# Performance work log

Hardware: AMD Instinct MI355X
Metric: run time of the kernel (lower is better)

The kernel has to match this reference:

```python
import jax, jax.numpy as jnp
import numpy as np

VOCAB = 50257
CH = 1024          # c_hidden_size = hidden_size(1020) + class_num(4)
LAT = 128
T = 1024
EOS = 1


def setup_inputs() -> dict:
    key = jax.random.key(0)
    ks = jax.random.split(key, 12)
    s = 0.02
    # tokens in [2, VOCAB) so EOS only appears at the final position
    toks = jax.random.randint(ks[0], (T,), 2, VOCAB, dtype=jnp.int32)
    input_tensor = toks.at[-1].set(EOS)
    inp = {
        "input_tensor": input_tensor,
        "h0": jnp.zeros((1, 1, CH), jnp.float32),
        "c0": jnp.zeros((1, 1, CH), jnp.float32),
        "eps": jax.random.normal(ks[1], (1, 1, LAT), jnp.float32),
        "emb": jax.random.normal(ks[2], (VOCAB, CH), jnp.float32) * s,
        "W_ih": jax.random.normal(ks[3], (4 * CH, CH), jnp.float32) * s,
        "W_hh": jax.random.normal(ks[4], (4 * CH, CH), jnp.float32) * s,
        "b_ih": jax.random.normal(ks[5], (4 * CH,), jnp.float32) * s,
        "b_hh": jax.random.normal(ks[6], (4 * CH,), jnp.float32) * s,
        "W_mean": jax.random.normal(ks[7], (LAT, 2 * CH), jnp.float32) * s,
        "b_mean": jnp.zeros((LAT,), jnp.float32),
        "W_logv": jax.random.normal(ks[8], (LAT, 2 * CH), jnp.float32) * s,
        "b_logv": jnp.zeros((LAT,), jnp.float32),
    }
    return inp


def reference(input_tensor, h0, c0, eps, emb, W_ih, W_hh, b_ih, b_hh,
              W_mean, b_mean, W_logv, b_logv):
    Tlen = input_tensor.shape[0]
    eos_idx = jnp.argmax(input_tensor == EOS)           # first EOS position
    active = jnp.arange(Tlen) < eos_idx                 # steps taken before break
    x_all = emb[input_tensor]                            # [T, CH]

    def step(carry, inp):
        h, c = carry
        x, a = inp
        gates = x @ W_ih.T + b_ih + h @ W_hh.T + b_hh    # [4*CH]
        i, f, g, o = jnp.split(gates, 4)                 # PyTorch LSTM gate order
        c_new = jax.nn.sigmoid(f) * c + jax.nn.sigmoid(i) * jnp.tanh(g)
        h_new = jax.nn.sigmoid(o) * jnp.tanh(c_new)
        h = jnp.where(a, h_new, h)
        c = jnp.where(a, c_new, c)
        return (h, c), None

    (h, c), _ = jax.lax.scan(step, (h0.reshape(-1), c0.reshape(-1)), (x_all, active))
    hc = jnp.concatenate([h, c])                         # cat((h, c), dim=2) flattened
    mean = hc @ W_mean.T + b_mean
    logv = hc @ W_logv.T + b_logv
    z = eps.reshape(-1) * jnp.exp(0.5 * logv) + mean     # reparameterize
    shp = (1, 1, LAT)
    return z.reshape(shp), mean.reshape(shp), logv.reshape(shp)
```

## Files before the change

### kernel.cpp

```cpp
#include <hip/hip_runtime.h>
#include <cstdint>
#include <cstddef>

#define T_LEN 1024
#define CH    1024
#define NGATE 4096
#define LAT   128
#define NBLK  128

#define WS_XG    0
#define WS_HBUF  (16777216)
#define WS_HFIN  (16777216 + 16384)
#define WS_CFIN  (16777216 + 24576)
#define WS_CTRL  (16777216 + 32768)

__device__ __forceinline__ float sigmf(float x) { return 1.0f / (1.0f + expf(-x)); }

__global__ __launch_bounds__(1024) void setup_k(const int* __restrict__ tok,
                                                int* __restrict__ ctrl) {
  __shared__ int red[1024];
  int tid = threadIdx.x;
  red[tid] = (tok[tid] == 1) ? tid : 0x7fffffff;
  __syncthreads();
  for (int s = 512; s > 0; s >>= 1) {
    if (tid < s) red[tid] = min(red[tid], red[tid + s]);
    __syncthreads();
  }
  if (tid == 0) {
    int e = red[0];
    ctrl[0] = (e == 0x7fffffff) ? 0 : e;
  }
}

__global__ __launch_bounds__(512) void xgemm_k(const int* __restrict__ tok,
                                               const float* __restrict__ emb,
                                               const float* __restrict__ Wih,
                                               const float* __restrict__ bih,
                                               const float* __restrict__ bhh,
                                               float* __restrict__ xg) {
  __shared__ float As[16 * 132];
  __shared__ float Bs[16 * 132];
  const int tid = threadIdx.x;
  const int r0 = blockIdx.x * 128;
  const int t0 = blockIdx.y * 128;
  const int tx = tid & 15, ty = tid >> 4;
  const int m0 = ty * 4, n0 = tx * 8;
  const int lrow = tid >> 2;
  const int kq   = (tid & 3) * 4;

  float acc[4][8];
#pragma unroll
  for (int i = 0; i < 4; i++)
#pragma unroll
    for (int j = 0; j < 8; j++) acc[i][j] = 0.0f;

  const int tokv = tok[t0 + lrow];
  const float* arow = emb + (size_t)tokv * CH;
  const float* brow = Wih + (size_t)(r0 + lrow) * CH;

  for (int k0 = 0; k0 < CH; k0 += 16) {
    float4 a4 = *(const float4*)(arow + k0 + kq);
    float4 b4 = *(const float4*)(brow + k0 + kq);
    __syncthreads();
    As[(kq + 0) * 132 + lrow] = a4.x;
    As[(kq + 1) * 132 + lrow] = a4.y;
    As[(kq + 2) * 132 + lrow] = a4.z;
    As[(kq + 3) * 132 + lrow] = a4.w;
    Bs[(kq + 0) * 132 + lrow] = b4.x;
    Bs[(kq + 1) * 132 + lrow] = b4.y;
    Bs[(kq + 2) * 132 + lrow] = b4.z;
    Bs[(kq + 3) * 132 + lrow] = b4.w;
    __syncthreads();
#pragma unroll
    for (int kk = 0; kk < 16; kk++) {
      float4 av = *(const float4*)&As[kk * 132 + m0];
      float4 b0 = *(const float4*)&Bs[kk * 132 + n0];
      float4 b1 = *(const float4*)&Bs[kk * 132 + n0 + 4];
      float aa[4] = {av.x, av.y, av.z, av.w};
      float bb[8] = {b0.x, b0.y, b0.z, b0.w, b1.x, b1.y, b1.z, b1.w};
#pragma unroll
      for (int i = 0; i < 4; i++)
#pragma unroll
        for (int j = 0; j < 8; j++) acc[i][j] += aa[i] * bb[j];
    }
  }

  float4 bi0 = *(const float4*)(bih + r0 + n0);
  float4 bi1 = *(const float4*)(bih + r0 + n0 + 4);
  float4 bh0 = *(const float4*)(bhh + r0 + n0);
  float4 bh1 = *(const float4*)(bhh + r0 + n0 + 4);
  float badd[8] = {bi0.x + bh0.x, bi0.y + bh0.y, bi0.z + bh0.z, bi0.w + bh0.w,
                   bi1.x + bh1.x, bi1.y + bh1.y, bi1.z + bh1.z, bi1.w + bh1.w};
#pragma unroll
  for (int i = 0; i < 4; i++) {
    float4 o0 = {acc[i][0] + badd[0], acc[i][1] + badd[1],
                 acc[i][2] + badd[2], acc[i][3] + badd[3]};
    float4 o1 = {acc[i][4] + badd[4], acc[i][5] + badd[5],
                 acc[i][6] + badd[6], acc[i][7] + badd[7]};
    float* dst = xg + (size_t)(t0 + m0 + i) * NGATE + r0 + n0;
    *(float4*)(dst) = o0;
    *(float4*)(dst + 4) = o1;
  }
}

__global__ __launch_bounds__(1024) void lstm_k(const float* __restrict__ h0,
                                               const float* __restrict__ c0,
                                               const float* __restrict__ eps,
                                               const float* __restrict__ Whh,
                                               const float* __restrict__ Wm,
                                               const float* __restrict__ bm,
                                               const float* __restrict__ Wl,
                                               const float* __restrict__ bl,
                                               const float* __restrict__ xg,
                                               unsigned long long* __restrict__ hbuf64,
                                               unsigned long long* __restrict__ hfin64,
                                               unsigned long long* __restrict__ cfin64,
                                               const int* __restrict__ ctrl,
                                               float* __restrict__ out) {
  __shared__ float hs[1024];
  __shared__ float hcs[2048];
  __shared__ float gv[32];
  __shared__ float rs[32];

  const int tid = threadIdx.x;
  const int b = blockIdx.x;
  const int g = tid >> 5, s = tid & 31;
  const int q = g >> 3, jj = g & 7;
  const int r = q * 1024 + b * 8 + jj;

  const float* wrow = Whh + (size_t)r * CH;
  float w[32];
#pragma unroll
  for (int i = 0; i < 32; i++) w[i] = wrow[s + 32 * i];

  const int eos = ctrl[0];

  float hreg = 0.0f, creg = 0.0f;
  if (tid < 8) { hreg = h0[b * 8 + tid]; creg = c0[b * 8 + tid]; }

  for (int t = 0; t < eos; t++) {
    float xv = 0.0f;
    if (s == 0) xv = xg[(size_t)t * NGATE + r];

    if (t == 0) {
      hs[tid] = h0[tid];
    } else {
      const unsigned want = (unsigned)t;
      const unsigned long long* src = hbuf64 + (size_t)(t & 1) * 1024 + tid;
      unsigned long long v;
      do {
        v = __hip_atomic_load(src, __ATOMIC_RELAXED, __HIP_MEMORY_SCOPE_AGENT);
      } while ((unsigned)(v >> 32) != want);
      hs[tid] = __uint_as_float((unsigned)(v & 0xffffffffu));
    }
    __syncthreads();

    float a0 = 0.0f, a1 = 0.0f;
#pragma unroll
    for (int i = 0; i < 32; i += 2) {
      a0 += w[i]     * hs[s + 32 * i];
      a1 += w[i + 1] * hs[s + 32 * (i + 1)];
    }
    float acc = a0 + a1;
    acc += __shfl_xor(acc, 16);
    acc += __shfl_xor(acc, 8);
    acc += __shfl_xor(acc, 4);
    acc += __shfl_xor(acc, 2);
    acc += __shfl_xor(acc, 1);
    if (s == 0) gv[g] = acc + xv;
    __syncthreads();

    if (tid < 8) {
      float iv = gv[tid], fv = gv[8 + tid], gg = gv[16 + tid], ov = gv[24 + tid];
      float cn = sigmf(fv) * creg + sigmf(iv) * tanhf(gg);
      float hn = sigmf(ov) * tanhf(cn);
      creg = cn; hreg = hn;
      unsigned long long pv = ((unsigned long long)(unsigned)(t + 1) << 32) |
                              (unsigned long long)__float_as_uint(hn);
      __hip_atomic_store(&hbuf64[(size_t)((t + 1) & 1) * 1024 + b * 8 + tid], pv,
                         __ATOMIC_RELAXED, __HIP_MEMORY_SCOPE_AGENT);
    }
  }

  if (tid < 8) {
    unsigned long long ph = (1ull << 32) | (unsigned long long)__float_as_uint(hreg);
    unsigned long long pc = (1ull << 32) | (unsigned long long)__float_as_uint(creg);
    __hip_atomic_store(&hfin64[b * 8 + tid], ph, __ATOMIC_RELAXED, __HIP_MEMORY_SCOPE_AGENT);
    __hip_atomic_store(&cfin64[b * 8 + tid], pc, __ATOMIC_RELAXED, __HIP_MEMORY_SCOPE_AGENT);
  }

  {
    unsigned long long vh, vc;
    do {
      vh = __hip_atomic_load(&hfin64[tid], __ATOMIC_RELAXED, __HIP_MEMORY_SCOPE_AGENT);
    } while ((unsigned)(vh >> 32) != 1u);
    do {
      vc = __hip_atomic_load(&cfin64[tid], __ATOMIC_RELAXED, __HIP_MEMORY_SCOPE_AGENT);
    } while ((unsigned)(vc >> 32) != 1u);
    hcs[tid] = __uint_as_float((unsigned)(vh & 0xffffffffu));
    hcs[1024 + tid] = __uint_as_float((unsigned)(vc & 0xffffffffu));
  }
  __syncthreads();

  float hc1 = hcs[tid];
  float hc2 = hcs[1024 + tid];
  float pm = Wm[(size_t)b * 2048 + tid] * hc1 + Wm[(size_t)b * 2048 + 1024 + tid] * hc2;
  float pl = Wl[(size_t)b * 2048 + tid] * hc1 + Wl[(size_t)b * 2048 + 1024 + tid] * hc2;
#pragma unroll
  for (int o = 32; o > 0; o >>= 1) {
    pm += __shfl_down(pm, o);
    pl += __shfl_down(pl, o);
  }
  const int wv = tid >> 6, ln = tid & 63;
  if (ln == 0) { rs[wv] = pm; rs[16 + wv] = pl; }
  __syncthreads();
  if (tid == 0) {
    float m = 0.0f, l = 0.0f;
    for (int i = 0; i < 16; i++) { m += rs[i]; l += rs[16 + i]; }
    m += bm[b];
    l += bl[b];
    float z = eps[b] * expf(0.5f * l) + m;
    out[b] = z;
    out[LAT + b] = m;
    out[2 * LAT + b] = l;
  }
}

extern "C" void kernel_launch(void* const* d_in, const int* in_sizes, int n_in,
                              void* d_out, int out_size, void* d_ws, size_t ws_size,
                              hipStream_t stream) {
  const int*   tok = (const int*)d_in[0];
  const float* h0  = (const float*)d_in[1];
  const float* c0  = (const float*)d_in[2];
  const float* eps = (const float*)d_in[3];
  const float* emb = (const float*)d_in[4];
  const float* Wih = (const float*)d_in[5];
  const float* Whh = (const float*)d_in[6];
  const float* bih = (const float*)d_in[7];
  const float* bhh = (const float*)d_in[8];
  const float* Wm  = (const float*)d_in[9];
  const float* bm  = (const float*)d_in[10];
  const float* Wl  = (const float*)d_in[11];
  const float* bl  = (const float*)d_in[12];
  float* out = (float*)d_out;

  char* ws = (char*)d_ws;
  float* xg = (float*)(ws + WS_XG);
  unsigned long long* hbuf64 = (unsigned long long*)(ws + WS_HBUF);
  unsigned long long* hfin64 = (unsigned long long*)(ws + WS_HFIN);
  unsigned long long* cfin64 = (unsigned long long*)(ws + WS_CFIN);
  int* ctrl = (int*)(ws + WS_CTRL);

  setup_k<<<1, 1024, 0, stream>>>(tok, ctrl);
  xgemm_k<<<dim3(NGATE / 128, T_LEN / 128), 512, 0, stream>>>(tok, emb, Wih, bih, bhh, xg);

  void* args[] = {(void*)&h0, (void*)&c0, (void*)&eps, (void*)&Whh,
                  (void*)&Wm, (void*)&bm, (void*)&Wl, (void*)&bl,
                  (void*)&xg, (void*)&hbuf64, (void*)&hfin64, (void*)&cfin64,
                  (void*)&ctrl, (void*)&out};
  hipLaunchCooperativeKernel((void*)lstm_k, dim3(NBLK), dim3(1024), args, 0, stream);
}
```

Baseline: 2.460 ms.

## Remap LSTM recurrence so each wave computes all four gates for one hidden unit

Restructures the per-step recurrent matvec so each of 8 waves per block owns one hidden unit and computes all four gate dot products with contiguous float4 weight registers. Gate sums use DPP row reductions instead of shuffle-xor, and the lane that holds the final sum applies the cell update directly. This removes the second __syncthreads and the gate shared-memory exchange. The h vector is double-buffered in swizzled LDS to avoid bank conflicts on float4 reads, and half the waves in each block sit idle during the loop.

```diff
diff --git a/kernel.cpp b/kernel.cpp
--- a/kernel.cpp
+++ b/kernel.cpp
@@ -14,7 +14,25 @@
 #define WS_CFIN  (16777216 + 24576)
 #define WS_CTRL  (16777216 + 32768)
 
+#define SWZ(i) ((i) ^ ((((i) >> 4) & 7) << 2))
+
 __device__ __forceinline__ float sigmf(float x) { return 1.0f / (1.0f + expf(-x)); }
+
+template <int CTRL, int RM>
+__device__ __forceinline__ float dpp_add(float x) {
+  int t = __builtin_amdgcn_update_dpp(0, __float_as_int(x), CTRL, RM, 0xf, true);
+  return x + __int_as_float(t);
+}
+
+__device__ __forceinline__ float wave_sum63(float x) {
+  x = dpp_add<0x111, 0xf>(x);
+  x = dpp_add<0x112, 0xf>(x);
+  x = dpp_add<0x114, 0xf>(x);
+  x = dpp_add<0x118, 0xf>(x);
+  x = dpp_add<0x142, 0xa>(x);
+  x = dpp_add<0x143, 0xc>(x);
+  return x;
+}
 
 __global__ __launch_bounds__(1024) void setup_k(const int* __restrict__ tok,
                                                 int* __restrict__ ctrl) {
@@ -117,76 +135,91 @@
                                                unsigned long long* __restrict__ cfin64,
                                                const int* __restrict__ ctrl,
                                                float* __restrict__ out) {
-  __shared__ float hs[1024];
+  __shared__ float hs[2][1024];
   __shared__ float hcs[2048];
-  __shared__ float gv[32];
   __shared__ float rs[32];
 
   const int tid = threadIdx.x;
   const int b = blockIdx.x;
-  const int g = tid >> 5, s = tid & 31;
-  const int q = g >> 3, jj = g & 7;
-  const int r = q * 1024 + b * 8 + jj;
-
-  const float* wrow = Whh + (size_t)r * CH;
-  float w[32];
-#pragma unroll
-  for (int i = 0; i < 32; i++) w[i] = wrow[s + 32 * i];
+  const int wv = tid >> 6;
+  const int ln = tid & 63;
+
+  float4 w4[4][4];
+  if (wv < 8) {
+#pragma unroll
+    for (int q = 0; q < 4; q++) {
+      const float* wr = Whh + (size_t)(q * 1024 + b * 8 + wv) * CH + ln * 16;
+#pragma unroll
+      for (int m = 0; m < 4; m++) w4[q][m] = *(const float4*)(wr + 4 * m);
+    }
+  }
 
   const int eos = ctrl[0];
 
   float hreg = 0.0f, creg = 0.0f;
-  if (tid < 8) { hreg = h0[b * 8 + tid]; creg = c0[b * 8 + tid]; }
+  if (wv < 8 && ln == 63) { hreg = h0[b * 8 + wv]; creg = c0[b * 8 + wv]; }
 
   for (int t = 0; t < eos; t++) {
-    float xv = 0.0f;
-    if (s == 0) xv = xg[(size_t)t * NGATE + r];
-
+    float xq0 = 0.0f, xq1 = 0.0f, xq2 = 0.0f, xq3 = 0.0f;
+    if (wv < 8 && ln == 63) {
+      const float* xp = xg + (size_t)t * NGATE + b * 8 + wv;
+      xq0 = xp[0]; xq1 = xp[1024]; xq2 = xp[2048]; xq3 = xp[3072];
+    }
+
+    const int pb = t & 1;
     if (t == 0) {
-      hs[tid] = h0[tid];
+      hs[0][SWZ(tid)] = h0[tid];
     } else {
       const unsigned want = (unsigned)t;
-      const unsigned long long* src = hbuf64 + (size_t)(t & 1) * 1024 + tid;
+      const unsigned long long* src = hbuf64 + (size_t)pb * 1024 + tid;
       unsigned long long v;
       do {
         v = __hip_atomic_load(src, __ATOMIC_RELAXED, __HIP_MEMORY_SCOPE_AGENT);
       } while ((unsigned)(v >> 32) != want);
-      hs[tid] = __uint_as_float((unsigned)(v & 0xffffffffu));
-    }
-    __syncthreads();
-
-    float a0 = 0.0f, a1 = 0.0f;
-#pragma unroll
-    for (int i = 0; i < 32; i += 2) {
-      a0 += w[i]     * hs[s + 32 * i];
-      a1 += w[i + 1] * hs[s + 32 * (i + 1)];
-    }
-    float acc = a0 + a1;
-    acc += __shfl_xor(acc, 16);
-    acc += __shfl_xor(acc, 8);
-    acc += __shfl_xor(acc, 4);
-    acc += __shfl_xor(acc, 2);
-    acc += __shfl_xor(acc, 1);
-    if (s == 0) gv[g] = acc + xv;
-    __syncthreads();
-
-    if (tid < 8) {
-      float iv = gv[tid], fv = gv[8 + tid], gg = gv[16 + tid], ov = gv[24 + tid];
-      float cn = sigmf(fv) * creg + sigmf(iv) * tanhf(gg);
-      float hn = sigmf(ov) * tanhf(cn);
-      creg = cn; hreg = hn;
-      unsigned long long pv = ((unsigned long long)(unsigned)(t + 1) << 32) |
-                              (unsigned long long)__float_as_uint(hn);
-      __hip_atomic_store(&hbuf64[(size_t)((t + 1) & 1) * 1024 + b * 8 + tid], pv,
-                         __ATOMIC_RELAXED, __HIP_MEMORY_SCOPE_AGENT);
-    }
-  }
-
-  if (tid < 8) {
-    unsigned long long ph = (1ull << 32) | (unsigned long long)__float_as_uint(hreg);
-    unsigned long long pc = (1ull << 32) | (unsigned long long)__float_as_uint(creg);
-    __hip_atomic_store(&hfin64[b * 8 + tid], ph, __ATOMIC_RELAXED, __HIP_MEMORY_SCOPE_AGENT);
-    __hip_atomic_store(&cfin64[b * 8 + tid], pc, __ATOMIC_RELAXED, __HIP_MEMORY_SCOPE_AGENT);
+      hs[pb][SWZ(tid)] = __uint_as_float((unsigned)(v & 0xffffffffu));
+    }
+    __syncthreads();
+
+    if (wv < 8) {
+      const float* hb = hs[pb];
+      float a0 = 0.0f, a1 = 0.0f, a2 = 0.0f, a3 = 0.0f;
+#pragma unroll
+      for (int m = 0; m < 4; m++) {
+        const int idx = (ln * 16 + 4 * m) ^ ((ln & 7) << 2);
+        const float4 h4 = *(const float4*)(hb + idx);
+        a0 += w4[0][m].x * h4.x; a0 += w4[0][m].y * h4.y;
+        a0 += w4[0][m].z * h4.z; a0 += w4[0][m].w * h4.w;
+        a1 += w4[1][m].x * h4.x; a1 += w4[1][m].y * h4.y;
+        a1 += w4[1][m].z * h4.z; a1 += w4[1][m].w * h4.w;
+        a2 += w4[2][m].x * h4.x; a2 += w4[2][m].y * h4.y;
+        a2 += w4[2][m].z * h4.z; a2 += w4[2][m].w * h4.w;
+        a3 += w4[3][m].x * h4.x; a3 += w4[3][m].y * h4.y;
+        a3 += w4[3][m].z * h4.z; a3 += w4[3][m].w * h4.w;
+      }
+      a0 = wave_sum63(a0);
+      a1 = wave_sum63(a1);
+      a2 = wave_sum63(a2);
+      a3 = wave_sum63(a3);
+
+      if (ln == 63) {
+        const float iv = a0 + xq0, fv = a1 + xq1, gg = a2 + xq2, ov = a3 + xq3;
+        const float cn = sigmf(fv) * creg + sigmf(iv) * tanhf(gg);
+        const float hn = sigmf(ov) * tanhf(cn);
+        creg = cn; hreg = hn;
+        const unsigned long long pv =
+            ((unsigned long long)(unsigned)(t + 1) << 32) |
+            (unsigned long long)__float_as_uint(hn);
+        __hip_atomic_store(&hbuf64[(size_t)((t + 1) & 1) * 1024 + b * 8 + wv], pv,
+                           __ATOMIC_RELAXED, __HIP_MEMORY_SCOPE_AGENT);
+      }
+    }
+  }
+
+  if (wv < 8 && ln == 63) {
+    const unsigned long long ph = (1ull << 32) | (unsigned long long)__float_as_uint(hreg);
+    const unsigned long long pc = (1ull << 32) | (unsigned long long)__float_as_uint(creg);
+    __hip_atomic_store(&hfin64[b * 8 + wv], ph, __ATOMIC_RELAXED, __HIP_MEMORY_SCOPE_AGENT);
+    __hip_atomic_store(&cfin64[b * 8 + wv], pc, __ATOMIC_RELAXED, __HIP_MEMORY_SCOPE_AGENT);
   }
 
   {
@@ -211,7 +244,6 @@
     pm += __shfl_down(pm, o);
     pl += __shfl_down(pl, o);
   }
-  const int wv = tid >> 6, ln = tid & 63;
   if (ln == 0) { rs[wv] = pm; rs[16 + wv] = pl; }
   __syncthreads();
   if (tid == 0) {
```

New measurement: 4.008 ms. 62.9% more time.
